# Kernel optimization log

Hardware: AMD Instinct MI355X
Metric: run time of the kernel (lower is better)

The kernel has to match this reference:

```python
import jax, jax.numpy as jnp
import numpy as np

B, T, D = 4, 4096, 1024
H, K, V = 16, 64, 64
EPS = 1e-6


def setup_inputs() -> dict:
    key = jax.random.key(0)
    ks = jax.random.split(key, 7)
    s = 0.02
    return {
        "x": jax.random.normal(ks[0], (B, T, D), dtype=jnp.float32),
        "norm_w": jnp.ones((D,), dtype=jnp.float32),
        "Wk": jax.random.normal(ks[1], (H * K, D), dtype=jnp.float32) * s,
        "Wv": jax.random.normal(ks[2], (H * V, D), dtype=jnp.float32) * s,
        "Wo": jax.random.normal(ks[3], (D, H * V), dtype=jnp.float32) * s,
        "Wb": jax.random.normal(ks[4], (H, D), dtype=jnp.float32) * s,
        "bb": jnp.full((H,), -2.0, dtype=jnp.float32),
        "Wg": jax.random.normal(ks[5], (H, D), dtype=jnp.float32) * s,
        "bg": jnp.full((H,), 2.0, dtype=jnp.float32),
    }


def reference(x, norm_w, Wk, Wv, Wo, Wb, bb, Wg, bg):
    # RMSNorm
    rms = jnp.sqrt(jnp.mean(x * x, axis=-1, keepdims=True) + EPS)
    xn = x / rms * norm_w  # [B,T,D]

    k = (xn @ Wk.T).reshape(B, T, H, K)
    v = (xn @ Wv.T).reshape(B, T, H, V)
    # L2-normalize keys (F.normalize, eps=1e-12)
    kn = jnp.linalg.norm(k, axis=-1, keepdims=True)
    k = k / jnp.maximum(kn, 1e-12)

    beta = jax.nn.sigmoid(xn @ Wb.T + bb)  # [B,T,H]
    g = jax.nn.sigmoid(xn @ Wg.T + bg)     # [B,T,H]

    # time-major for scan
    k_t = jnp.transpose(k, (1, 0, 2, 3))       # [T,B,H,K]
    v_t = jnpp = jnp.transpose(v, (1, 0, 2, 3))  # [T,B,H,V]
    b_t = jnp.transpose(beta, (1, 0, 2))       # [T,B,H]
    g_t = jnp.transpose(g, (1, 0, 2))          # [T,B,H]

    state0 = jnp.zeros((B, H, K, V), dtype=jnp.float32)

    def step(state, inp):
        kt, vt, bt, gt = inp  # [B,H,K],[B,H,V],[B,H],[B,H]
        pred = jnp.einsum('bhkv,bhk->bhv', state, kt)
        err = vt - pred
        state = gt[..., None, None] * state + bt[..., None, None] * (kt[..., :, None] * err[..., None, :])
        out_t = jnp.einsum('bhkv,bhk->bhv', state, kt)
        return state, out_t

    final_state, out = jax.lax.scan(step, state0, (k_t, v_t, b_t, g_t))
    out = jnp.transpose(out, (1, 0, 2, 3)).reshape(B, T, H * V)  # [B,T,H*V]
    y = x + out @ Wo.T
    return y
```

## Files before the change

kernel.cpp:

```cpp
#include <hip/hip_runtime.h>
#include <stdint.h>

#define B_ 4
#define T_ 4096
#define D_ 1024
#define H_ 16
#define NPAD 2304
#define ROWS (B_*T_)

typedef __bf16 bf16x8 __attribute__((ext_vector_type(8)));
typedef float  f32x4  __attribute__((ext_vector_type(4)));
typedef unsigned short u16;
typedef u16 u16x8 __attribute__((ext_vector_type(8)));
typedef u16 u16x4 __attribute__((ext_vector_type(4)));

__device__ __forceinline__ float bf2f(u16 u){
  union { unsigned int i; float f; } x; x.i = ((unsigned int)u) << 16; return x.f;
}
__device__ __forceinline__ u16 f2bf(float f){
  union { float f; unsigned int i; } x; x.f = f;
  unsigned int r = x.i + 0x7fffu + ((x.i >> 16) & 1u);
  return (u16)(r >> 16);
}
__device__ __forceinline__ bf16x8 as_bf(u16x8 v){ union{u16x8 u; bf16x8 b;} x; x.u = v; return x.b; }

__device__ __forceinline__ void gload_lds16(const u16* g, u16* l){
  __builtin_amdgcn_global_load_lds(
      (const __attribute__((address_space(1))) unsigned int*)g,
      (__attribute__((address_space(3))) unsigned int*)l, 16, 0, 0);
}

__global__ __launch_bounds__(256) void prep_w(
    const float* __restrict__ Wk, const float* __restrict__ Wv,
    const float* __restrict__ Wb, const float* __restrict__ Wg,
    const float* __restrict__ Wo, u16* __restrict__ Wcomb, u16* __restrict__ Wob)
{
  long i = (long)blockIdx.x * 256 + threadIdx.x;
  const long tot1 = (long)NPAD * D_;
  if (i < tot1) {
    long n = i >> 10, d = i & 1023;
    float v;
    if      (n < 1024) v = Wk[n * 1024 + d];
    else if (n < 2048) v = Wv[(n - 1024) * 1024 + d];
    else if (n < 2064) v = Wb[(n - 2048) * 1024 + d];
    else if (n < 2080) v = Wg[(n - 2064) * 1024 + d];
    else               v = 0.f;
    Wcomb[i] = f2bf(v);
  } else {
    long j = i - tot1;
    Wob[j] = f2bf(Wo[j]);
  }
}

__global__ __launch_bounds__(256) void rmsnorm_k(
    const float* __restrict__ x, const float* __restrict__ w, u16* __restrict__ xn)
{
  long row = blockIdx.x;
  int tid = threadIdx.x;
  int l = tid & 63, wv = tid >> 6;
  f32x4 v = ((const f32x4*)(x + row * D_))[tid];
  float ss = v[0]*v[0] + v[1]*v[1] + v[2]*v[2] + v[3]*v[3];
  #pragma unroll
  for (int m = 1; m < 64; m <<= 1) ss += __shfl_xor(ss, m, 64);
  __shared__ float red[4];
  if (l == 0) red[wv] = ss;
  __syncthreads();
  float tot = red[0] + red[1] + red[2] + red[3];
  float inv = rsqrtf(tot * (1.f / (float)D_) + 1e-6f);
  f32x4 wv4 = ((const f32x4*)w)[tid];
  u16x4 o;
  o[0] = f2bf(v[0] * inv * wv4[0]);
  o[1] = f2bf(v[1] * inv * wv4[1]);
  o[2] = f2bf(v[2] * inv * wv4[2]);
  o[3] = f2bf(v[3] * inv * wv4[3]);
  ((u16x4*)(xn + row * D_))[tid] = o;
}

extern __shared__ f32x4 lds_dyn[];

template<int RESID, int OUTF32>
__global__ __launch_bounds__(512, 2) void gemm256(
    const u16* __restrict__ A, const u16* __restrict__ Bm,
    u16* __restrict__ Cb, float* __restrict__ Cf, const float* __restrict__ resid,
    int M, int N, int Kd)
{
  const int tid = threadIdx.x;
  const int w = tid >> 6, l = tid & 63;
  const int lm = l & 15, lq = l >> 4;
  const int wm = w >> 2, wn = w & 3;

  unsigned gx = gridDim.x;
  unsigned bid = blockIdx.y * gx + blockIdx.x;
  unsigned nwg = gx * gridDim.y;
  unsigned cpx = nwg >> 3;
  unsigned swz = (bid & 7) * cpx + (bid >> 3);
  const long bm0 = (long)(swz / gx) * 256;
  const long bn0 = (long)(swz % gx) * 256;

  char* lds = (char*)lds_dyn;

  int rowS[2];
  #pragma unroll
  for (int r = 0; r < 2; ++r) rowS[r] = r*128 + w*16 + (l >> 2);
  const int colS = ((l & 3) ^ ((l >> 3) & 3)) * 8;

  auto STAGE_A = [&](int t, int q){
    char* base = lds + q*32768;
    long k0 = (long)t * 32;
    #pragma unroll
    for (int r = 0; r < 2; ++r)
      gload_lds16(A + (bm0 + rowS[r])*(long)Kd + k0 + colS,
                  (u16*)(base + (r*512 + w*64)*16));
  };
  auto STAGE_B = [&](int t, int q){
    char* base = lds + q*32768 + 16384;
    long k0 = (long)t * 32;
    #pragma unroll
    for (int r = 0; r < 2; ++r)
      gload_lds16(Bm + (bn0 + rowS[r])*(long)Kd + k0 + colS,
                  (u16*)(base + (r*512 + w*64)*16));
  };

  const unsigned soff = (unsigned)(lq ^ ((lm >> 1) & 3)) << 4;

  f32x4 acc[8][4];
  #pragma unroll
  for (int i = 0; i < 8; ++i)
    #pragma unroll
    for (int j = 0; j < 4; ++j) acc[i][j] = f32x4{0.f,0.f,0.f,0.f};

  const int NT = Kd >> 5;
  STAGE_A(0, 0); STAGE_B(0, 0);
  STAGE_A(1, 1); STAGE_B(1, 1);

  for (int t = 0; t < NT; ++t) {
    int q  = t % 3;
    int qn = (t + 2) % 3;
    int tn = (t + 2 < NT) ? (t + 2) : (NT - 1);

    asm volatile("s_waitcnt vmcnt(4)" ::: "memory");
    __builtin_amdgcn_s_barrier();
    asm volatile("" ::: "memory");

    const char* Ab = lds + q*32768;
    const char* Bb = Ab + 16384;

    bf16x8 bfr[4], afr[8];
    #pragma unroll
    for (int nf = 0; nf < 4; ++nf) {
      int rr = wn*64 + nf*16 + lm;
      bfr[nf] = *(const bf16x8*)(Bb + rr*64 + soff);
    }
    #pragma unroll
    for (int mf = 0; mf < 8; ++mf) {
      int rr = wm*128 + mf*16 + lm;
      afr[mf] = *(const bf16x8*)(Ab + rr*64 + soff);
    }
    STAGE_A(tn, qn);
    STAGE_B(tn, qn);

    __builtin_amdgcn_s_setprio(1);
    #pragma unroll
    for (int mf = 0; mf < 8; ++mf)
      #pragma unroll
      for (int nf = 0; nf < 4; ++nf)
        acc[mf][nf] = __builtin_amdgcn_mfma_f32_16x16x32_bf16(afr[mf], bfr[nf], acc[mf][nf], 0, 0, 0);
    __builtin_amdgcn_s_setprio(0);
  }

  #pragma unroll
  for (int mf = 0; mf < 8; ++mf) {
    #pragma unroll
    for (int r = 0; r < 4; ++r) {
      long m = bm0 + wm*128 + mf*16 + lq*4 + r;
      #pragma unroll
      for (int nf = 0; nf < 4; ++nf) {
        long n = bn0 + wn*64 + nf*16 + lm;
        float val = acc[mf][nf][r];
        if (RESID) val += resid[m * N + n];
        if (OUTF32) Cf[m * N + n] = val;
        else        Cb[m * N + n] = f2bf(val);
      }
    }
  }
}

template<int RESID, int OUTF32>
__global__ __launch_bounds__(256) void gemm_nt(
    const u16* __restrict__ A, const u16* __restrict__ Bm,
    u16* __restrict__ Cb, float* __restrict__ Cf, const float* __restrict__ resid,
    int M, int N, int Kd)
{
  __shared__ __align__(16) u16 Als[128 * 32];
  __shared__ __align__(16) u16 Bls[128 * 32];
  const int tid = threadIdx.x;
  const int w = tid >> 6, l = tid & 63;
  const int wr = w >> 1, wc = w & 1;
  const int lm = l & 15, lq = l >> 4;

  unsigned bid = blockIdx.y * gridDim.x + blockIdx.x;
  unsigned nwg = gridDim.x * gridDim.y;
  unsigned cpx = nwg >> 3;
  unsigned swz = (bid & 7) * cpx + (bid >> 3);
  const long bm0 = (long)(swz / gridDim.x) * 128;
  const long bn0 = (long)(swz % gridDim.x) * 128;

  f32x4 zero4 = {0.f, 0.f, 0.f, 0.f};
  f32x4 acc[4][4];
  #pragma unroll
  for (int i = 0; i < 4; i++)
    #pragma unroll
    for (int j = 0; j < 4; j++) acc[i][j] = zero4;

  for (int kk = 0; kk < Kd; kk += 32) {
    __syncthreads();
    #pragma unroll
    for (int it = 0; it < 2; it++) {
      int c = tid + it * 256;
      int r = c >> 2, kb = c & 3;
      const u16* ga = A  + (bm0 + r) * Kd + kk + kb * 8;
      const u16* gb = Bm + (bn0 + r) * Kd + kk + kb * 8;
      gload_lds16(ga, Als + (it * 256 + w * 64) * 8);
      gload_lds16(gb, Bls + (it * 256 + w * 64) * 8);
    }
    __syncthreads();
    bf16x8 af[4], bfr[4];
    #pragma unroll
    for (int f = 0; f < 4; f++)
      af[f] = *(const bf16x8*)(Als + (wr * 64 + f * 16 + lm) * 32 + lq * 8);
    #pragma unroll
    for (int f = 0; f < 4; f++)
      bfr[f] = *(const bf16x8*)(Bls + (wc * 64 + f * 16 + lm) * 32 + lq * 8);
    #pragma unroll
    for (int i = 0; i < 4; i++)
      #pragma unroll
      for (int j = 0; j < 4; j++)
        acc[i][j] = __builtin_amdgcn_mfma_f32_16x16x32_bf16(af[i], bfr[j], acc[i][j], 0, 0, 0);
  }

  #pragma unroll
  for (int i = 0; i < 4; i++) {
    #pragma unroll
    for (int r = 0; r < 4; r++) {
      long m = bm0 + wr * 64 + i * 16 + lq * 4 + r;
      #pragma unroll
      for (int j = 0; j < 4; j++) {
        long n = bn0 + wc * 64 + j * 16 + lm;
        float val = acc[i][j][r];
        if (RESID) val += resid[m * N + n];
        if (OUTF32) Cf[m * N + n] = val;
        else        Cb[m * N + n] = f2bf(val);
      }
    }
  }
}

__global__ __launch_bounds__(64) void postproc(
    u16* __restrict__ kv, const float* __restrict__ bb, const float* __restrict__ bg,
    float* __restrict__ bArr, float* __restrict__ gArr)
{
  long row = blockIdx.x;
  int l = threadIdx.x;
  u16* rp = kv + row * NPAD;
  #pragma unroll
  for (int h = 0; h < 16; h++) {
    float xk = bf2f(rp[h * 64 + l]);
    float ss = xk * xk;
    #pragma unroll
    for (int m = 1; m < 64; m <<= 1) ss += __shfl_xor(ss, m, 64);
    float inv = 1.f / fmaxf(sqrtf(ss), 1e-12f);
    rp[h * 64 + l] = f2bf(xk * inv);
  }
  if (l < 32) {
    int hh = l & 15;
    float val = bf2f(rp[2048 + l]) + ((l < 16) ? bb[hh] : bg[hh]);
    float s = 1.f / (1.f + expf(-val));
    float* dst = (l < 16) ? bArr : gArr;
    long b = row >> 12;
    long t = row & 4095;
    dst[(b * H_ + hh) * (long)T_ + t] = s;
  }
}

__device__ __forceinline__ void mm64(const u16* Ab, const u16* Bb,
                                     int lm, int lq, int wr, int wc, f32x4 acc[2][2])
{
  #pragma unroll
  for (int ks = 0; ks < 2; ++ks) {
    bf16x8 af[2], bfr[2];
    #pragma unroll
    for (int mi = 0; mi < 2; ++mi)
      af[mi] = *(const bf16x8*)(Ab + (wr*32 + mi*16 + lm)*72 + ks*32 + lq*8);
    #pragma unroll
    for (int ni = 0; ni < 2; ++ni)
      bfr[ni] = *(const bf16x8*)(Bb + (wc*32 + ni*16 + lm)*72 + ks*32 + lq*8);
    #pragma unroll
    for (int mi = 0; mi < 2; ++mi)
      #pragma unroll
      for (int ni = 0; ni < 2; ++ni)
        acc[mi][ni] = __builtin_amdgcn_mfma_f32_16x16x32_bf16(af[mi], bfr[ni], acc[mi][ni], 0, 0, 0);
  }
}

__global__ __launch_bounds__(256) void chunk1(
    u16* __restrict__ kv, const float* __restrict__ bArr, const float* __restrict__ gArr,
    u16* __restrict__ p1buf, u16* __restrict__ r1buf)
{
  __shared__ __align__(16) u16 Kb[64*72];
  __shared__ __align__(16) u16 Utb[128*72];
  __shared__ __align__(16) u16 LpI[64*72];
  __shared__ __align__(16) u16 Abf[64*72];
  __shared__ __align__(16) float Ad[4*16*21];
  __shared__ float aLS[64], ainvLS[64], bLS[64], bapLS[64];
  __shared__ float aCsh;

  const int tid = threadIdx.x;
  const int w = tid >> 6, l = tid & 63;
  const int lm = l & 15, lq = l >> 4;
  const int wr = w >> 1, wc = w & 1;
  const int bh = blockIdx.x & 63, ch = blockIdx.x >> 6;
  const int b = bh >> 4, h = bh & 15;

  const u16* kbase = kv + ((long)b*T_ + ch*64)*NPAD + h*64;
  const u16* vbase = kbase + 1024;

  #pragma unroll
  for (int it = 0; it < 2; ++it) {
    int c = tid + it*256;
    int r = c >> 3, seg = (c & 7)*8;
    *(u16x8*)(Kb  + r*72 + seg) = *(const u16x8*)(kbase + (long)r*NPAD + seg);
    *(u16x8*)(Utb + r*72 + seg) = *(const u16x8*)(vbase + (long)r*NPAD + seg);
  }
  #pragma unroll
  for (int z = 0; z < 8; ++z) {
    int idx = tid + z*256;
    int rr = idx >> 5, wd = idx & 31;
    ((unsigned int*)(Utb + (64 + rr)*72))[wd] = 0u;
  }
  if (tid < 64) {
    float gv = gArr[(long)bh*T_ + ch*64 + tid];
    float bv = bArr[(long)bh*T_ + ch*64 + tid];
    float av = gv;
    #pragma unroll
    for (int off = 1; off < 64; off <<= 1) {
      float o = __shfl_up(av, off, 64);
      if (tid >= off) av *= o;
    }
    float ap = __shfl_up(av, 1, 64);
    if (tid == 0) ap = 1.f;
    float aC = __shfl(av, 63, 64);
    aLS[tid] = av; ainvLS[tid] = 1.f/av; bLS[tid] = bv; bapLS[tid] = bv*ap;
    if (tid == 0) aCsh = aC;
  }
  __syncthreads();

  f32x4 gf[2][2];
  #pragma unroll
  for (int mi = 0; mi < 2; ++mi)
    #pragma unroll
    for (int ni = 0; ni < 2; ++ni) gf[mi][ni] = f32x4{0.f,0.f,0.f,0.f};
  mm64(Kb, Kb, lm, lq, wr, wc, gf);

  float wv_[4][2][4];
  #pragma unroll
  for (int bi = 0; bi < 4; ++bi)
    #pragma unroll
    for (int ni = 0; ni < 2; ++ni) {
      int col = w*32 + ni*16 + lm;
      #pragma unroll
      for (int r = 0; r < 4; ++r) {
        int row = bi*16 + lq*4 + r;
        float sv = (col < 64) ? bf2f(Utb[row*72 + col]) : bf2f(Kb[row*72 + (col - 64)]);
        float coef = (col < 64) ? bLS[row] : bapLS[row];
        wv_[bi][ni][r] = coef * sv;
      }
    }

  #pragma unroll
  for (int mi = 0; mi < 2; ++mi)
    #pragma unroll
    for (int ni = 0; ni < 2; ++ni)
      #pragma unroll
      for (int r = 0; r < 4; ++r) {
        int row = wr*32 + mi*16 + lq*4 + r, col = wc*32 + ni*16 + lm;
        float gvl = gf[mi][ni][r];
        int rb = row >> 4, cb = col >> 4;
        Abf[row*72 + col] = f2bf((rb > cb) ? bapLS[row]*ainvLS[col]*gvl : 0.f);
        if (rb == cb)
          Ad[(rb*16 + (row & 15))*21 + (col & 15)] =
              ((col & 15) < (row & 15)) ? bapLS[row]*ainvLS[col]*gvl : 0.f;
        LpI[row*72 + col] = f2bf((col < row) ? aLS[row]*ainvLS[col]*gvl
                                             : ((col == row) ? 1.f : 0.f));
      }
  __syncthreads();

  #pragma unroll
  for (int bi = 0; bi < 4; ++bi) {
    if (bi > 0) {
      f32x4 corr[2] = { f32x4{0.f,0.f,0.f,0.f}, f32x4{0.f,0.f,0.f,0.f} };
      const int nks = (bi*16 + 31) >> 5;
      #pragma unroll
      for (int ks = 0; ks < 2; ++ks) {
        if (ks < nks) {
          bf16x8 afr = *(const bf16x8*)(Abf + (bi*16 + lm)*72 + ks*32 + lq*8);
          #pragma unroll
          for (int ni = 0; ni < 2; ++ni) {
            bf16x8 bfr = *(const bf16x8*)(Utb + (w*32 + ni*16 + lm)*72 + ks*32 + lq*8);
            corr[ni] = __builtin_amdgcn_mfma_f32_16x16x32_bf16(afr, bfr, corr[ni], 0, 0, 0);
          }
        }
      }
      #pragma unroll
      for (int ni = 0; ni < 2; ++ni)
        #pragma unroll
        for (int r = 0; r < 4; ++r) wv_[bi][ni][r] -= corr[ni][r];
    }
    #pragma unroll
    for (int i = 0; i < 16; ++i) {
      int src = ((i >> 2) << 4) | lm;
      float u0 = __shfl(wv_[bi][0][i & 3], src, 64);
      float u1 = __shfl(wv_[bi][1][i & 3], src, 64);
      #pragma unroll
      for (int r = 0; r < 4; ++r) {
        float ad = Ad[(bi*16 + lq*4 + r)*21 + i];
        wv_[bi][0][r] = fmaf(-ad, u0, wv_[bi][0][r]);
        wv_[bi][1][r] = fmaf(-ad, u1, wv_[bi][1][r]);
      }
    }
    #pragma unroll
    for (int ni = 0; ni < 2; ++ni) {
      int col = w*32 + ni*16 + lm;
      #pragma unroll
      for (int r = 0; r < 4; ++r)
        Utb[col*72 + bi*16 + lq*4 + r] = f2bf(wv_[bi][ni][r]);
    }
  }
  __syncthreads();

  const long pr_base = (((long)bh*64 + ch)*64);
  u16* qdst = kv + ((long)b*T_ + ch*64)*NPAD + h*64;
  u16* mdst = qdst + 1024;
  f32x4 acc[2][2];

  #pragma unroll
  for (int mi = 0; mi < 2; ++mi)
    #pragma unroll
    for (int ni = 0; ni < 2; ++ni) acc[mi][ni] = f32x4{0.f,0.f,0.f,0.f};
  mm64(Utb, LpI, lm, lq, wr, wc, acc);
  #pragma unroll
  for (int mi = 0; mi < 2; ++mi)
    #pragma unroll
    for (int ni = 0; ni < 2; ++ni)
      #pragma unroll
      for (int r = 0; r < 4; ++r) {
        int row = wr*32 + mi*16 + lq*4 + r, col = wc*32 + ni*16 + lm;
        p1buf[(pr_base + row)*64 + col] = f2bf(acc[mi][ni][r]);
      }

  #pragma unroll
  for (int mi = 0; mi < 2; ++mi)
    #pragma unroll
    for (int ni = 0; ni < 2; ++ni) acc[mi][ni] = f32x4{0.f,0.f,0.f,0.f};
  mm64(LpI, Utb + 64*72, lm, lq, wr, wc, acc);
  #pragma unroll
  for (int mi = 0; mi < 2; ++mi)
    #pragma unroll
    for (int ni = 0; ni < 2; ++ni)
      #pragma unroll
      for (int r = 0; r < 4; ++r) {
        int row = wr*32 + mi*16 + lq*4 + r, col = wc*32 + ni*16 + lm;
        float val = aLS[row]*bf2f(Kb[row*72 + col]) - acc[mi][ni][r];
        qdst[(long)row*NPAD + col] = f2bf(val);
      }

  {
    int kk_ = tid >> 2, sb = (tid & 3) * 16;
    float aC = aCsh;
    #pragma unroll
    for (int s5 = 0; s5 < 16; ++s5) {
      int s = sb + s5;
      Abf[kk_*72 + s] = f2bf(aC * ainvLS[s] * bf2f(Kb[s*72 + kk_]));
    }
  }
  __syncthreads();

  #pragma unroll
  for (int mi = 0; mi < 2; ++mi)
    #pragma unroll
    for (int ni = 0; ni < 2; ++ni) acc[mi][ni] = f32x4{0.f,0.f,0.f,0.f};
  mm64(Utb, Abf, lm, lq, wr, wc, acc);
  #pragma unroll
  for (int mi = 0; mi < 2; ++mi)
    #pragma unroll
    for (int ni = 0; ni < 2; ++ni)
      #pragma unroll
      for (int r = 0; r < 4; ++r) {
        int row = wr*32 + mi*16 + lq*4 + r, col = wc*32 + ni*16 + lm;
        r1buf[(pr_base + row)*64 + col] = f2bf(acc[mi][ni][r]);
      }

  #pragma unroll
  for (int mi = 0; mi < 2; ++mi)
    #pragma unroll
    for (int ni = 0; ni < 2; ++ni) acc[mi][ni] = f32x4{0.f,0.f,0.f,0.f};
  mm64(Abf, Utb + 64*72, lm, lq, wr, wc, acc);
  #pragma unroll
  for (int mi = 0; mi < 2; ++mi)
    #pragma unroll
    for (int ni = 0; ni < 2; ++ni)
      #pragma unroll
      for (int r = 0; r < 4; ++r) {
        int row = wr*32 + mi*16 + lq*4 + r, col = wc*32 + ni*16 + lm;
        float val = ((row == col) ? aCsh : 0.f) - acc[mi][ni][r];
        mdst[(long)row*NPAD + col] = f2bf(val);
      }
}

struct PF { u16x8 qf0, qf1, mf0, mf1; u16 p1[4]; u16 r1[4]; };

__global__ __launch_bounds__(256) void chunk2(
    const u16* __restrict__ kv, const u16* __restrict__ p1buf, const u16* __restrict__ r1buf,
    u16* __restrict__ outb)
{
  __shared__ __align__(16) u16 Zb[16*72];
  __shared__ __align__(16) u16 ot[64*24];
  const int tid = threadIdx.x;
  const int wcv = tid >> 6, l = tid & 63;
  const int lm = l & 15, lq = l >> 4;
  const int bh = blockIdx.x & 63, vg = blockIdx.x >> 6;
  const int b = bh >> 4, h = bh & 15;

  for (int idx = tid; idx < 16*72/2; idx += 256) ((unsigned int*)Zb)[idx] = 0u;

  const u16* pbase = p1buf + (long)bh*64*4096;
  const u16* rbase = r1buf + (long)bh*64*4096;

  auto LOADPF = [&](int ch, PF& p){
    long rq = ((long)b*T_ + ch*64 + wcv*16 + lm)*NPAD + h*64 + lq*8;
    p.qf0 = *(const u16x8*)(kv + rq);
    p.qf1 = *(const u16x8*)(kv + rq + 32);
    p.mf0 = *(const u16x8*)(kv + rq + 1024);
    p.mf1 = *(const u16x8*)(kv + rq + 1024 + 32);
    #pragma unroll
    for (int r = 0; r < 4; ++r) {
      long pv = (long)ch*4096 + (vg*16 + lq*4 + r)*64 + wcv*16 + lm;
      p.p1[r] = pbase[pv];
      p.r1[r] = rbase[pv];
    }
  };

  PF A, Bp;
  LOADPF(0, A);
  __syncthreads();

  auto STEP = [&](int ch, PF& use, PF& pre){
    bf16x8 za0 = *(const bf16x8*)(Zb + lm*72 + lq*8);
    bf16x8 za1 = *(const bf16x8*)(Zb + lm*72 + 32 + lq*8);
    if (ch < 63) LOADPF(ch + 1, pre);
    f32x4 accO = { bf2f(use.p1[0]), bf2f(use.p1[1]), bf2f(use.p1[2]), bf2f(use.p1[3]) };
    accO = __builtin_amdgcn_mfma_f32_16x16x32_bf16(za0, as_bf(use.qf0), accO, 0, 0, 0);
    accO = __builtin_amdgcn_mfma_f32_16x16x32_bf16(za1, as_bf(use.qf1), accO, 0, 0, 0);
    f32x4 accS = { bf2f(use.r1[0]), bf2f(use.r1[1]), bf2f(use.r1[2]), bf2f(use.r1[3]) };
    accS = __builtin_amdgcn_mfma_f32_16x16x32_bf16(za0, as_bf(use.mf0), accS, 0, 0, 0);
    accS = __builtin_amdgcn_mfma_f32_16x16x32_bf16(za1, as_bf(use.mf1), accS, 0, 0, 0);
    #pragma unroll
    for (int r = 0; r < 4; ++r) ot[(wcv*16 + lm)*24 + lq*4 + r] = f2bf(accO[r]);
    __syncthreads();
    #pragma unroll
    for (int r = 0; r < 4; ++r) Zb[(lq*4 + r)*72 + wcv*16 + lm] = f2bf(accS[r]);
    {
      int i2 = tid >> 2, q4 = tid & 3;
      u16x4 ov = *(const u16x4*)(ot + i2*24 + q4*4);
      *(u16x4*)(outb + ((long)b*T_ + ch*64 + i2)*D_ + h*64 + vg*16 + q4*4) = ov;
    }
    __syncthreads();
  };

  for (int c2 = 0; c2 < 32; ++c2) {
    STEP(2*c2,     A, Bp);
    STEP(2*c2 + 1, Bp, A);
  }
}

extern "C" void kernel_launch(void* const* d_in, const int* in_sizes, int n_in,
                              void* d_out, int out_size, void* d_ws, size_t ws_size,
                              hipStream_t stream) {
  const float* x     = (const float*)d_in[0];
  const float* normw = (const float*)d_in[1];
  const float* Wk    = (const float*)d_in[2];
  const float* Wv    = (const float*)d_in[3];
  const float* Wo    = (const float*)d_in[4];
  const float* Wb    = (const float*)d_in[5];
  const float* bb    = (const float*)d_in[6];
  const float* Wg    = (const float*)d_in[7];
  const float* bg    = (const float*)d_in[8];
  float* y = (float*)d_out;

  char* ws = (char*)d_ws;
  u16* xn    = (u16*)ws;   ws += (long)ROWS * D_ * 2;
  u16* Wcomb = (u16*)ws;   ws += (long)NPAD * D_ * 2;
  u16* Wob   = (u16*)ws;   ws += (long)D_ * D_ * 2;
  u16* kvb   = (u16*)ws;   ws += (long)ROWS * NPAD * 2;
  float* bA  = (float*)ws; ws += (long)B_ * H_ * T_ * 4;
  float* gA  = (float*)ws; ws += (long)B_ * H_ * T_ * 4;
  u16* outb  = (u16*)ws;   ws += (long)ROWS * D_ * 2;
  u16* r1b   = (u16*)ws;   ws += (long)64 * 64 * 4096 * 2;

  const int LDSB = 3 * 32768;
  bool big = true;
  if (hipFuncSetAttribute(reinterpret_cast<const void*>(gemm256<0,0>),
        hipFuncAttributeMaxDynamicSharedMemorySize, LDSB) != hipSuccess) big = false;
  if (hipFuncSetAttribute(reinterpret_cast<const void*>(gemm256<1,1>),
        hipFuncAttributeMaxDynamicSharedMemorySize, LDSB) != hipSuccess) big = false;

  const long prep_total = (long)NPAD * D_ + (long)D_ * D_;
  prep_w<<<dim3((unsigned)(prep_total / 256)), dim3(256), 0, stream>>>(
      Wk, Wv, Wb, Wg, Wo, Wcomb, Wob);
  rmsnorm_k<<<dim3(ROWS), dim3(256), 0, stream>>>(x, normw, xn);
  if (big)
    gemm256<0, 0><<<dim3(NPAD / 256, ROWS / 256), dim3(512), LDSB, stream>>>(
        xn, Wcomb, kvb, (float*)nullptr, (const float*)nullptr, ROWS, NPAD, D_);
  else
    gemm_nt<0, 0><<<dim3(NPAD / 128, ROWS / 128), dim3(256), 0, stream>>>(
        xn, Wcomb, kvb, (float*)nullptr, (const float*)nullptr, ROWS, NPAD, D_);
  postproc<<<dim3(ROWS), dim3(64), 0, stream>>>(kvb, bb, bg, bA, gA);
  chunk1<<<dim3(4096), dim3(256), 0, stream>>>(kvb, bA, gA, xn, r1b);
  chunk2<<<dim3(256), dim3(256), 0, stream>>>(kvb, xn, r1b, outb);
  if (big)
    gemm256<1, 1><<<dim3(D_ / 256, ROWS / 256), dim3(512), LDSB, stream>>>(
        outb, Wob, (u16*)nullptr, y, x, ROWS, D_, D_);
  else
    gemm_nt<1, 1><<<dim3(D_ / 128, ROWS / 128), dim3(256), 0, stream>>>(
        outb, Wob, (u16*)nullptr, y, x, ROWS, D_, D_);
}
```

Baseline: 348.7 us.

## Fold key L2-normalization into chunk kernel via Gram diagonal scaling

Drops the per-row key normalization pass that rewrote the whole key block in global memory. The squared norms are now read from the diagonal of the K·Kᵀ Gram product already computed in chunk1, and the inverse norms are folded into the per-row coefficients. The remaining sigmoid work moves to a slimmer elementwise kernel with 256-thread blocks. Two smaller changes ride along: the diagonal-block triangular coefficients are stored as bf16 and read with vector loads, and the transposed Abf build is remapped. Risks are lower precision in the triangular solve coefficients and the Gram product now running on unnormalized bf16 keys.

```diff
diff --git a/kernel.cpp b/kernel.cpp
--- a/kernel.cpp
+++ b/kernel.cpp
@@ -255,31 +255,18 @@
   }
 }
 
-__global__ __launch_bounds__(64) void postproc(
-    u16* __restrict__ kv, const float* __restrict__ bb, const float* __restrict__ bg,
+__global__ __launch_bounds__(256) void sigmoid_bg(
+    const u16* __restrict__ kv, const float* __restrict__ bb, const float* __restrict__ bg,
     float* __restrict__ bArr, float* __restrict__ gArr)
 {
-  long row = blockIdx.x;
-  int l = threadIdx.x;
-  u16* rp = kv + row * NPAD;
-  #pragma unroll
-  for (int h = 0; h < 16; h++) {
-    float xk = bf2f(rp[h * 64 + l]);
-    float ss = xk * xk;
-    #pragma unroll
-    for (int m = 1; m < 64; m <<= 1) ss += __shfl_xor(ss, m, 64);
-    float inv = 1.f / fmaxf(sqrtf(ss), 1e-12f);
-    rp[h * 64 + l] = f2bf(xk * inv);
-  }
-  if (l < 32) {
-    int hh = l & 15;
-    float val = bf2f(rp[2048 + l]) + ((l < 16) ? bb[hh] : bg[hh]);
-    float s = 1.f / (1.f + expf(-val));
-    float* dst = (l < 16) ? bArr : gArr;
-    long b = row >> 12;
-    long t = row & 4095;
-    dst[(b * H_ + hh) * (long)T_ + t] = s;
-  }
+  int idx = blockIdx.x * 256 + threadIdx.x;
+  int row = idx >> 5, c = idx & 31;
+  int h = c & 15;
+  float val = bf2f(kv[(long)row * NPAD + 2048 + c]) + ((c < 16) ? bb[h] : bg[h]);
+  float s = 1.f / (1.f + expf(-val));
+  long b = row >> 12, t = row & 4095;
+  float* dst = (c < 16) ? bArr : gArr;
+  dst[(b * H_ + h) * (long)T_ + t] = s;
 }
 
 __device__ __forceinline__ void mm64(const u16* Ab, const u16* Bb,
@@ -310,7 +297,8 @@
   __shared__ __align__(16) u16 Utb[128*72];
   __shared__ __align__(16) u16 LpI[64*72];
   __shared__ __align__(16) u16 Abf[64*72];
-  __shared__ __align__(16) float Ad[4*16*21];
+  __shared__ __align__(16) u16 Adb[4*16*24];
+  __shared__ float nrm2LS[64];
   __shared__ float aLS[64], ainvLS[64], bLS[64], bapLS[64];
   __shared__ float aCsh;
 
@@ -361,6 +349,22 @@
     for (int ni = 0; ni < 2; ++ni) gf[mi][ni] = f32x4{0.f,0.f,0.f,0.f};
   mm64(Kb, Kb, lm, lq, wr, wc, gf);
 
+  #pragma unroll
+  for (int mi = 0; mi < 2; ++mi)
+    #pragma unroll
+    for (int ni = 0; ni < 2; ++ni)
+      #pragma unroll
+      for (int r = 0; r < 4; ++r) {
+        int row = wr*32 + mi*16 + lq*4 + r, col = wc*32 + ni*16 + lm;
+        if (row == col) nrm2LS[row] = gf[mi][ni][r];
+      }
+  __syncthreads();
+  if (tid < 64) {
+    float nv = 1.f / fmaxf(sqrtf(nrm2LS[tid]), 1e-12f);
+    aLS[tid] *= nv; ainvLS[tid] *= nv; bapLS[tid] *= nv;
+  }
+  __syncthreads();
+
   float wv_[4][2][4];
   #pragma unroll
   for (int bi = 0; bi < 4; ++bi)
@@ -387,8 +391,8 @@
         int rb = row >> 4, cb = col >> 4;
         Abf[row*72 + col] = f2bf((rb > cb) ? bapLS[row]*ainvLS[col]*gvl : 0.f);
         if (rb == cb)
-          Ad[(rb*16 + (row & 15))*21 + (col & 15)] =
-              ((col & 15) < (row & 15)) ? bapLS[row]*ainvLS[col]*gvl : 0.f;
+          Adb[rb*384 + (row & 15)*24 + (col & 15)] =
+              f2bf(((col & 15) < (row & 15)) ? bapLS[row]*ainvLS[col]*gvl : 0.f);
         LpI[row*72 + col] = f2bf((col < row) ? aLS[row]*ainvLS[col]*gvl
                                              : ((col == row) ? 1.f : 0.f));
       }
@@ -415,6 +419,12 @@
         #pragma unroll
         for (int r = 0; r < 4; ++r) wv_[bi][ni][r] -= corr[ni][r];
     }
+    u16x8 ad0[4], ad1[4];
+    #pragma unroll
+    for (int r = 0; r < 4; ++r) {
+      ad0[r] = *(const u16x8*)(Adb + bi*384 + (lq*4 + r)*24);
+      ad1[r] = *(const u16x8*)(Adb + bi*384 + (lq*4 + r)*24 + 8);
+    }
     #pragma unroll
     for (int i = 0; i < 16; ++i) {
       int src = ((i >> 2) << 4) | lm;
@@ -422,7 +432,7 @@
       float u1 = __shfl(wv_[bi][1][i & 3], src, 64);
       #pragma unroll
       for (int r = 0; r < 4; ++r) {
-        float ad = Ad[(bi*16 + lq*4 + r)*21 + i];
+        float ad = bf2f((i < 8) ? ad0[r][i] : ad1[r][i - 8]);
         wv_[bi][0][r] = fmaf(-ad, u0, wv_[bi][0][r]);
         wv_[bi][1][r] = fmaf(-ad, u1, wv_[bi][1][r]);
       }
@@ -474,13 +484,11 @@
       }
 
   {
-    int kk_ = tid >> 2, sb = (tid & 3) * 16;
-    float aC = aCsh;
-    #pragma unroll
-    for (int s5 = 0; s5 < 16; ++s5) {
-      int s = sb + s5;
-      Abf[kk_*72 + s] = f2bf(aC * ainvLS[s] * bf2f(Kb[s*72 + kk_]));
-    }
+    int s = tid & 63, kk0 = (tid >> 6) * 16;
+    float coef = aCsh * ainvLS[s];
+    #pragma unroll
+    for (int j = 0; j < 16; ++j)
+      Abf[(kk0 + j)*72 + s] = f2bf(coef * bf2f(Kb[s*72 + kk0 + j]));
   }
   __syncthreads();
 
@@ -623,7 +631,7 @@
   else
     gemm_nt<0, 0><<<dim3(NPAD / 128, ROWS / 128), dim3(256), 0, stream>>>(
         xn, Wcomb, kvb, (float*)nullptr, (const float*)nullptr, ROWS, NPAD, D_);
-  postproc<<<dim3(ROWS), dim3(64), 0, stream>>>(kvb, bb, bg, bA, gA);
+  sigmoid_bg<<<dim3(ROWS * 32 / 256), dim3(256), 0, stream>>>(kvb, bb, bg, bA, gA);
   chunk1<<<dim3(4096), dim3(256), 0, stream>>>(kvb, bA, gA, xn, r1b);
   chunk2<<<dim3(256), dim3(256), 0, stream>>>(kvb, xn, r1b, outb);
   if (big)
```

Result: faster. 321.0 us (-7.9%).
